# Kernel optimization log

Measured on AMD Instinct MI355X. Metric: run time of the kernel, lower is better.

The kernel has to match this reference:

```python
import jax, jax.numpy as jnp
import numpy as np

B, C, H, W = 2, 256, 64, 64
HEADS = 8
HEAD_DIM = C // HEADS  # 32
INNER = HEADS * HEAD_DIM  # 256
GROUPS = 32
EPS = 1e-5


def groupnorm(x, w, b):
    # x: [B, C, H, W]; normalize over (C//G, H, W) within each of G groups
    Bx, Cx, Hx, Wx = x.shape
    xg = x.reshape(Bx, GROUPS, -1)
    mu = xg.mean(axis=-1, keepdims=True)
    var = xg.var(axis=-1, keepdims=True)
    xn = ((xg - mu) * jax.lax.rsqrt(var + EPS)).reshape(Bx, Cx, Hx, Wx)
    return xn * w[:, None, None] + b[:, None, None]


def setup_inputs() -> dict:
    key = jax.random.key(0)
    k0, k1, k2 = jax.random.split(key, 3)
    x = jax.random.normal(k0, (B, C, H, W), dtype=jnp.float32)
    gn_weight = jnp.ones((C,), dtype=jnp.float32)
    gn_bias = jnp.zeros((C,), dtype=jnp.float32)
    # 1x1 conv weights (kernel dims squeezed): [out_ch, in_ch]
    w_qkv = jax.random.normal(k1, (3 * INNER, C), dtype=jnp.float32) * 0.02
    w_out = jax.random.normal(k2, (C, INNER), dtype=jnp.float32) * 0.02
    return {"x": x, "gn_weight": gn_weight, "gn_bias": gn_bias,
            "w_qkv": w_qkv, "w_out": w_out}


def reference(x, gn_weight, gn_bias, w_qkv, w_out):
    Bx, Cx, Hx, Wx = x.shape
    N = Hx * Wx
    scale = HEAD_DIM ** -0.5
    xn = groupnorm(x, gn_weight, gn_bias)
    # 1x1 conv == channel matmul
    qkv = jnp.einsum('oc,bchw->bohw', w_qkv, xn)  # [B, 3*INNER, H, W]
    q, k, v = jnp.split(qkv, 3, axis=1)
    # 'b (h d) x y -> b h (x y) d'
    def to_heads(t):
        return t.reshape(Bx, HEADS, HEAD_DIM, N).transpose(0, 1, 3, 2)  # bhnd
    q, k, v = to_heads(q), to_heads(k), to_heads(v)
    sim = jnp.einsum('bhid,bhjd->bhij', q, k) * scale  # [B, h, N, N]
    attn = jax.nn.softmax(sim, axis=-1)
    o = jnp.einsum('bhij,bhjd->bhid', attn, v)  # [B, h, N, d]
    # 'b h (x y) d -> b (h d) x y'
    o = o.transpose(0, 1, 3, 2).reshape(Bx, INNER, Hx, Wx)
    out = jnp.einsum('co,bohw->bchw', w_out, o)
    return x + out
```

## Files before the change

### kernel.cpp

```cpp
#include <hip/hip_runtime.h>
#include <hip/hip_bf16.h>

#define BATCH 2
#define CH 256
#define HW 4096
#define HEADS 8
#define HDIM 32
#define GROUPS 32
#define EPS 1e-5f
#define SCALE 0.17677669529663687f
#define QSCALE (0.17677669529663687f * 1.4426950408889634f)

typedef short s16x8 __attribute__((ext_vector_type(8)));
typedef float floatx4 __attribute__((ext_vector_type(4)));
typedef unsigned short ushort_t;
typedef unsigned int uint_t;

static __device__ __forceinline__ ushort_t f2bf(float f) {
    __hip_bfloat16 h = __float2bfloat16(f);
    return *reinterpret_cast<ushort_t*>(&h);
}
static __device__ __forceinline__ float bf2f(uint_t u) {
    return __uint_as_float(u << 16);
}

static __device__ __forceinline__ uint_t pk2(float lo, float hi) {
    return __builtin_amdgcn_perm(__float_as_uint(hi), __float_as_uint(lo), 0x07060302u);
}

static __device__ __forceinline__ void gload_lds16(const ushort_t* g, ushort_t* l) {
    __builtin_amdgcn_global_load_lds((const __attribute__((address_space(1))) void*)g,
                                     (__attribute__((address_space(3))) void*)l, 16, 0, 0);
}

__global__ void gn_stats_wcvt(const float* __restrict__ x, float* __restrict__ stats,
                              const float* __restrict__ wq, const float* __restrict__ wo,
                              ushort_t* __restrict__ wdst) {
    if (blockIdx.x >= 64) {
        int i = (blockIdx.x - 64) * 256 + threadIdx.x;
        float4 v = (i < 49152) ? ((const float4*)wq)[i] : ((const float4*)wo)[i - 49152];
        ushort_t p[4] = {f2bf(v.x), f2bf(v.y), f2bf(v.z), f2bf(v.w)};
        uint2 o;
        o.x = (uint_t)p[0] | ((uint_t)p[1] << 16);
        o.y = (uint_t)p[2] | ((uint_t)p[3] << 16);
        *(uint2*)&wdst[(size_t)i * 4] = o;
        return;
    }
    int bg = blockIdx.x;
    const float4* xv = (const float4*)(x + (size_t)bg * 8 * HW);
    int t = threadIdx.x;
    float s = 0.f, ss = 0.f;
    for (int i = t; i < 8192; i += 256) {
        float4 v = xv[i];
        s  += v.x + v.y + v.z + v.w;
        ss += v.x*v.x + v.y*v.y + v.z*v.z + v.w*v.w;
    }
    #pragma unroll
    for (int off = 32; off; off >>= 1) {
        s  += __shfl_down(s, off);
        ss += __shfl_down(ss, off);
    }
    __shared__ float rs[4], rss[4];
    int wave = t >> 6;
    if ((t & 63) == 0) { rs[wave] = s; rss[wave] = ss; }
    __syncthreads();
    if (t == 0) {
        s  = rs[0] + rs[1] + rs[2] + rs[3];
        ss = rss[0] + rss[1] + rss[2] + rss[3];
        float mu  = s / 32768.f;
        float var = ss / 32768.f - mu * mu;
        stats[bg * 2]     = mu;
        stats[bg * 2 + 1] = rsqrtf(var + EPS);
    }
}

__global__ void norm_transpose(const float* __restrict__ x, const float* __restrict__ stats,
                               const float* __restrict__ gw, const float* __restrict__ gb,
                               ushort_t* __restrict__ xn) {
    __shared__ ushort_t tile[64][40];
    int b = blockIdx.z, c0 = blockIdx.y * 32, n0 = blockIdx.x * 64;
    int t = threadIdx.x;
    #pragma unroll
    for (int i = 0; i < 8; i++) {
        int idx = i * 256 + t;
        int c = idx >> 6, n = idx & 63;
        int cc = c0 + c;
        float mu   = stats[(b * GROUPS + (cc >> 3)) * 2];
        float rstd = stats[(b * GROUPS + (cc >> 3)) * 2 + 1];
        float v = x[((size_t)b * CH + cc) * HW + n0 + n];
        v = (v - mu) * rstd * gw[cc] + gb[cc];
        tile[n][c] = f2bf(v);
    }
    __syncthreads();
    int n = t >> 2, chk = t & 3;
    uint4 val = *(const uint4*)&tile[n][chk * 8];
    *(uint4*)(xn + ((size_t)(b * HW + n0 + n)) * CH + c0 + chk * 8) = val;
}

__global__ void qkv_gemm(const ushort_t* __restrict__ xn, const ushort_t* __restrict__ wqb,
                         ushort_t* __restrict__ qo, ushort_t* __restrict__ ko,
                         ushort_t* __restrict__ vo) {
    __shared__ ushort_t Al[64][40];
    __shared__ ushort_t Bl[128][40];
    int b = blockIdx.z;
    int n0 = blockIdx.x * 64, o0 = blockIdx.y * 128;
    int t = threadIdx.x, lane = t & 63, wave = t >> 6;
    int lr = lane & 15, lk = lane >> 4;
    int row = t >> 2, chk = t & 3;
    const ushort_t* asrc = xn + ((size_t)(b * HW + n0 + row)) * CH + chk * 8;
    int s1 = t + 256;
    const ushort_t* bsrc0 = wqb + (size_t)(o0 + (t >> 2)) * CH + (t & 3) * 8;
    const ushort_t* bsrc1 = wqb + (size_t)(o0 + (s1 >> 2)) * CH + (s1 & 3) * 8;
    floatx4 acc[8] = {};
    uint4 ra  = *(const uint4*)(asrc);
    uint4 rb0 = *(const uint4*)(bsrc0);
    uint4 rb1 = *(const uint4*)(bsrc1);
    for (int k0 = 0; k0 < 8; k0++) {
        *(uint4*)&Al[row][chk * 8] = ra;
        *(uint4*)&Bl[t >> 2][(t & 3) * 8] = rb0;
        *(uint4*)&Bl[s1 >> 2][(s1 & 3) * 8] = rb1;
        __syncthreads();
        if (k0 < 7) {
            ra  = *(const uint4*)(asrc + (k0 + 1) * 32);
            rb0 = *(const uint4*)(bsrc0 + (k0 + 1) * 32);
            rb1 = *(const uint4*)(bsrc1 + (k0 + 1) * 32);
        }
        s16x8 af = *(const s16x8*)&Al[wave * 16 + lr][lk * 8];
        #pragma unroll
        for (int ct = 0; ct < 8; ct++) {
            s16x8 bf = *(const s16x8*)&Bl[ct * 16 + lr][lk * 8];
            acc[ct] = __builtin_amdgcn_mfma_f32_16x16x32_bf16(af, bf, acc[ct], 0, 0, 0);
        }
        __syncthreads();
    }
    #pragma unroll
    for (int ct = 0; ct < 8; ct++) {
        int o = o0 + ct * 16 + lr;
        int sel = o >> 8;
        int h = (o >> 5) & 7;
        int d = o & 31;
        int nrow0 = n0 + wave * 16 + (lk << 2);
        if (sel == 0) {
            #pragma unroll
            for (int r = 0; r < 4; r++)
                qo[(((size_t)(b * HEADS + h)) * HW + nrow0 + r) * HDIM + d] =
                    f2bf(acc[ct][r] * QSCALE);
        } else if (sel == 1) {
            #pragma unroll
            for (int r = 0; r < 4; r++) {
                int tt = (nrow0 + r) & 63;
                int sg = 4 * ((tt >> 3) & 3) + 16 * ((((tt >> 2) & 1) << 1) | ((tt >> 5) & 1)) + (tt & 3);
                ko[(((size_t)(b * HEADS + h)) * HW + n0 + sg) * HDIM + d] = f2bf(acc[ct][r]);
            }
        } else {
            ushort_t pk[4];
            #pragma unroll
            for (int r = 0; r < 4; r++) pk[r] = f2bf(acc[ct][r]);
            *(uint2*)&vo[(((size_t)(b * HEADS + h)) * HDIM + d) * HW + nrow0] = *(uint2*)pk;
        }
    }
}

__global__ void __launch_bounds__(256, 4)
attn13(const ushort_t* __restrict__ qg, const ushort_t* __restrict__ kg,
       const ushort_t* __restrict__ vg, ushort_t* __restrict__ op0,
       ushort_t* __restrict__ op1, float* __restrict__ lpart) {
    __shared__ ushort_t Kl[2][2048];
    __shared__ ushort_t Vl[2][2048];
    const int bh = blockIdx.y;
    const int z = blockIdx.z;
    const int n0 = blockIdx.x * 128;
    const int t = threadIdx.x;
    const int lane = t & 63, w = t >> 6;
    const int lr = lane & 15, lk = lane >> 4;

    const ushort_t* kb = kg + (size_t)bh * HW * HDIM + (size_t)z * 1024 * HDIM;
    const ushort_t* vb = vg + (size_t)bh * HDIM * HW + z * 1024;

    const int lrr = t & 15, lkk = (t >> 4) & 3, wv = t >> 6;
    const ushort_t* gk = kb + ((wv << 4) + lrr) * HDIM + lkk * 8;
    const ushort_t* gv = vb + (size_t)(((t >> 7) << 4) + lrr) * HW + ((t >> 6) & 1) * 32 + lkk * 8;
    ushort_t* kd0 = &Kl[0][wv << 9]; ushort_t* kd1 = &Kl[1][wv << 9];
    ushort_t* vd0 = &Vl[0][wv << 9]; ushort_t* vd1 = &Vl[1][wv << 9];

    s16x8 qf0 = *(const s16x8*)(qg + ((size_t)bh * HW + n0 + w * 16 + lr) * HDIM + lk * 8);
    s16x8 qf1 = *(const s16x8*)(qg + ((size_t)bh * HW + n0 + 64 + w * 16 + lr) * HDIM + lk * 8);

    const s16x8 onesf = {0x3F80, 0x3F80, 0x3F80, 0x3F80, 0x3F80, 0x3F80, 0x3F80, 0x3F80};
    const floatx4 zf = {};
    floatx4 oacc[2][2] = {};
    floatx4 Lacc[2] = {};

    auto stage = [&](ushort_t* kdn, ushort_t* vdn) {
        gload_lds16(gk, kdn);
        gload_lds16(gv, vdn);
        gk += 64 * HDIM; gv += 64;
    };
    auto compute = [&](const ushort_t* Kb, const ushort_t* Vb) {
        floatx4 sim0[4], sim1[4];
        __builtin_amdgcn_s_setprio(1);
#pragma unroll
        for (int ct = 0; ct < 4; ct++) {
            s16x8 kf = *(const s16x8*)(Kb + ct * 512 + lane * 8);
            sim0[ct] = __builtin_amdgcn_mfma_f32_16x16x32_bf16(kf, qf0, zf, 0, 0, 0);
            sim1[ct] = __builtin_amdgcn_mfma_f32_16x16x32_bf16(kf, qf1, zf, 0, 0, 0);
        }
        __builtin_amdgcn_s_setprio(0);
        s16x8 vf[4];
#pragma unroll
        for (int i = 0; i < 4; i++)
            vf[i] = *(const s16x8*)(Vb + i * 512 + lane * 8);
        {
            s16x8 pf[2];
#pragma unroll
            for (int s = 0; s < 2; s++) {
                union { uint_t u[4]; s16x8 v; } pu;
                pu.u[0] = pk2(__builtin_amdgcn_exp2f(sim0[s][0]),     __builtin_amdgcn_exp2f(sim0[s][1]));
                pu.u[1] = pk2(__builtin_amdgcn_exp2f(sim0[s][2]),     __builtin_amdgcn_exp2f(sim0[s][3]));
                pu.u[2] = pk2(__builtin_amdgcn_exp2f(sim0[s + 2][0]), __builtin_amdgcn_exp2f(sim0[s + 2][1]));
                pu.u[3] = pk2(__builtin_amdgcn_exp2f(sim0[s + 2][2]), __builtin_amdgcn_exp2f(sim0[s + 2][3]));
                pf[s] = pu.v;
            }
            __builtin_amdgcn_s_setprio(1);
#pragma unroll
            for (int s = 0; s < 2; s++) {
                oacc[0][0] = __builtin_amdgcn_mfma_f32_16x16x32_bf16(vf[s],     pf[s], oacc[0][0], 0, 0, 0);
                oacc[0][1] = __builtin_amdgcn_mfma_f32_16x16x32_bf16(vf[2 + s], pf[s], oacc[0][1], 0, 0, 0);
                Lacc[0]    = __builtin_amdgcn_mfma_f32_16x16x32_bf16(onesf,     pf[s], Lacc[0],    0, 0, 0);
            }
            __builtin_amdgcn_s_setprio(0);
        }
        {
            s16x8 pf[2];
#pragma unroll
            for (int s = 0; s < 2; s++) {
                union { uint_t u[4]; s16x8 v; } pu;
                pu.u[0] = pk2(__builtin_amdgcn_exp2f(sim1[s][0]),     __builtin_amdgcn_exp2f(sim1[s][1]));
                pu.u[1] = pk2(__builtin_amdgcn_exp2f(sim1[s][2]),     __builtin_amdgcn_exp2f(sim1[s][3]));
                pu.u[2] = pk2(__builtin_amdgcn_exp2f(sim1[s + 2][0]), __builtin_amdgcn_exp2f(sim1[s + 2][1]));
                pu.u[3] = pk2(__builtin_amdgcn_exp2f(sim1[s + 2][2]), __builtin_amdgcn_exp2f(sim1[s + 2][3]));
                pf[s] = pu.v;
            }
            __builtin_amdgcn_s_setprio(1);
#pragma unroll
            for (int s = 0; s < 2; s++) {
                oacc[1][0] = __builtin_amdgcn_mfma_f32_16x16x32_bf16(vf[s],     pf[s], oacc[1][0], 0, 0, 0);
                oacc[1][1] = __builtin_amdgcn_mfma_f32_16x16x32_bf16(vf[2 + s], pf[s], oacc[1][1], 0, 0, 0);
                Lacc[1]    = __builtin_amdgcn_mfma_f32_16x16x32_bf16(onesf,     pf[s], Lacc[1],    0, 0, 0);
            }
            __builtin_amdgcn_s_setprio(0);
        }
    };

    stage(kd0, vd0);
    __syncthreads();
    for (int s2 = 0; s2 < 8; s2++) {
        stage(kd1, vd1);
        compute(&Kl[0][0], &Vl[0][0]);
        __syncthreads();
        if (s2 < 7) {
            stage(kd0, vd0);
            compute(&Kl[1][0], &Vl[1][0]);
            __syncthreads();
        } else {
            compute(&Kl[1][0], &Vl[1][0]);
        }
    }

    ushort_t* ob = (z == 0 ? op0 : op1 + (size_t)(z - 1) * 2097152) + ((size_t)bh * HW) * 32;
    float* lp = lpart + (size_t)(z * 16 + bh) * HW;
#pragma unroll
    for (int c = 0; c < 2; c++) {
        int n = n0 + c * 64 + w * 16 + lr;
        if (lk == 0) lp[n] = Lacc[c][0];
#pragma unroll
        for (int ct2 = 0; ct2 < 2; ct2++) {
            uint_t lo = (uint_t)f2bf(oacc[c][ct2][0]) | ((uint_t)f2bf(oacc[c][ct2][1]) << 16);
            uint_t hi = (uint_t)f2bf(oacc[c][ct2][2]) | ((uint_t)f2bf(oacc[c][ct2][3]) << 16);
            uint2 val = {lo, hi};
            *(uint2*)(ob + (size_t)n * 32 + ct2 * 16 + lk * 4) = val;
        }
    }
}

__global__ void attn_merge(const ushort_t* __restrict__ op0, const ushort_t* __restrict__ op1,
                           const float* __restrict__ lpart, ushort_t* __restrict__ oa) {
    int idx = blockIdx.x * 256 + threadIdx.x;
    int chunk = idx & 3;
    int n = (idx >> 2) & 4095;
    int bh = idx >> 14;
    size_t base = ((size_t)bh * HW + n) * 32 + chunk * 8;
    uint4 a0 = *(const uint4*)(op0 + base);
    uint4 a1 = *(const uint4*)(op1 + base);
    uint4 a2 = *(const uint4*)(op1 + 2097152 + base);
    uint4 a3 = *(const uint4*)(op1 + 2 * 2097152 + base);
    float L = lpart[(size_t)bh * HW + n] + lpart[(size_t)(16 + bh) * HW + n] +
              lpart[(size_t)(32 + bh) * HW + n] + lpart[(size_t)(48 + bh) * HW + n];
    float inv = 1.0f / L;
    uint_t u0[4] = {a0.x, a0.y, a0.z, a0.w}, u1[4] = {a1.x, a1.y, a1.z, a1.w};
    uint_t u2[4] = {a2.x, a2.y, a2.z, a2.w}, u3[4] = {a3.x, a3.y, a3.z, a3.w};
    ushort_t res[8];
#pragma unroll
    for (int i = 0; i < 4; i++) {
        float lo = bf2f(u0[i] & 0xffffu) + bf2f(u1[i] & 0xffffu) +
                   bf2f(u2[i] & 0xffffu) + bf2f(u3[i] & 0xffffu);
        float hi = bf2f(u0[i] >> 16) + bf2f(u1[i] >> 16) +
                   bf2f(u2[i] >> 16) + bf2f(u3[i] >> 16);
        res[2 * i]     = f2bf(lo * inv);
        res[2 * i + 1] = f2bf(hi * inv);
    }
    ushort_t* dst = oa + ((size_t)((bh >> 3) * HW) + n) * CH + (bh & 7) * 32 + chunk * 8;
    *(uint4*)dst = *(uint4*)res;
}

__global__ void proj_res(const ushort_t* __restrict__ oa, const ushort_t* __restrict__ wob,
                         const float* __restrict__ x, float* __restrict__ out) {
    __shared__ ushort_t Al[64][40];
    __shared__ ushort_t Bl[64][40];
    int m0 = blockIdx.x * 64;
    int c0 = blockIdx.y * 64;
    int t = threadIdx.x, lane = t & 63, wave = t >> 6;
    int lr = lane & 15, lk = lane >> 4;
    int row = t >> 2, chk = t & 3;
    const ushort_t* asrc = oa + (size_t)(m0 + row) * CH + chk * 8;
    const ushort_t* bsrc = wob + (size_t)(c0 + row) * CH + chk * 8;
    floatx4 acc[4] = {};
    uint4 ra = *(const uint4*)(asrc);
    uint4 rb = *(const uint4*)(bsrc);
    for (int k0 = 0; k0 < 8; k0++) {
        *(uint4*)&Al[row][chk * 8] = ra;
        *(uint4*)&Bl[row][chk * 8] = rb;
        __syncthreads();
        if (k0 < 7) {
            ra = *(const uint4*)(asrc + (k0 + 1) * 32);
            rb = *(const uint4*)(bsrc + (k0 + 1) * 32);
        }
        s16x8 af = *(const s16x8*)&Al[wave * 16 + lr][lk * 8];
        #pragma unroll
        for (int ct = 0; ct < 4; ct++) {
            s16x8 bf = *(const s16x8*)&Bl[ct * 16 + lr][lk * 8];
            acc[ct] = __builtin_amdgcn_mfma_f32_16x16x32_bf16(af, bf, acc[ct], 0, 0, 0);
        }
        __syncthreads();
    }
    int mrow0 = m0 + wave * 16 + (lk << 2);
    int b = mrow0 >> 12;
    int n = mrow0 & 4095;
    #pragma unroll
    for (int ct = 0; ct < 4; ct++) {
        int c = c0 + ct * 16 + lr;
        const float4 xv = *(const float4*)(x + ((size_t)(b * CH + c)) * HW + n);
        float4 ov;
        ov.x = acc[ct][0] + xv.x;
        ov.y = acc[ct][1] + xv.y;
        ov.z = acc[ct][2] + xv.z;
        ov.w = acc[ct][3] + xv.w;
        *(float4*)(out + ((size_t)(b * CH + c)) * HW + n) = ov;
    }
}

extern "C" void kernel_launch(void* const* d_in, const int* in_sizes, int n_in,
                              void* d_out, int out_size, void* d_ws, size_t ws_size,
                              hipStream_t stream) {
    const float* x    = (const float*)d_in[0];
    const float* gw   = (const float*)d_in[1];
    const float* gb   = (const float*)d_in[2];
    const float* wqkv = (const float*)d_in[3];
    const float* wout = (const float*)d_in[4];
    float* out = (float*)d_out;

    char* ws = (char*)d_ws;
    float* stats = (float*)ws;
    ushort_t* xn = (ushort_t*)(ws + 512);
    size_t per = (size_t)BATCH * HW * CH;
    ushort_t* q   = xn + per;
    ushort_t* k   = q + per;
    ushort_t* v   = k + per;
    ushort_t* oa  = v + per;
    ushort_t* wqb = oa + per;
    ushort_t* wob = wqb + 196608;
    ushort_t* op1 = wob + 65536;
    float* lpart  = (float*)(op1 + 3 * 2097152);
    ushort_t* op0 = xn;

    gn_stats_wcvt<<<320, 256, 0, stream>>>(x, stats, wqkv, wout, wqb);
    norm_transpose<<<dim3(64, 8, 2), 256, 0, stream>>>(x, stats, gw, gb, xn);
    qkv_gemm<<<dim3(64, 6, 2), 256, 0, stream>>>(xn, wqb, q, k, v);
    attn13<<<dim3(32, 16, 4), 256, 0, stream>>>(q, k, v, op0, op1, lpart);
    attn_merge<<<1024, 256, 0, stream>>>(op0, op1, lpart, oa);
    proj_res<<<dim3(128, 4), 256, 0, stream>>>(oa, wob, x, out);
}
```

Baseline: 85.02 us.

## Software-pipeline QK^T of next tile with softmax and PV of previous tile

Splits the attention inner step into a consume phase (QK^T MFMAs plus the V fragment loads from LDS) and a softmaxPV phase (exp2, packing, PV MFMAs). The loop is restructured so the QK^T for one K/V tile is issued while the exp and PV work of the previous tile is still pending. The intent is to overlap the transcendental ALU work with matrix-core work inside a wave. Keeping two sets of sim and V fragments raises register pressure, so launch bounds drop from 4 to 3 blocks per SIMD, which costs occupancy.

```diff
diff --git a/kernel.cpp b/kernel.cpp
--- a/kernel.cpp
+++ b/kernel.cpp
@@ -161,8 +161,8 @@
     }
 }
 
-__global__ void __launch_bounds__(256, 4)
-attn13(const ushort_t* __restrict__ qg, const ushort_t* __restrict__ kg,
+__global__ void __launch_bounds__(256, 3)
+attn14(const ushort_t* __restrict__ qg, const ushort_t* __restrict__ kg,
        const ushort_t* __restrict__ vg, ushort_t* __restrict__ op0,
        ushort_t* __restrict__ op1, float* __restrict__ lpart) {
     __shared__ ushort_t Kl[2][2048];
@@ -190,82 +190,71 @@
     const floatx4 zf = {};
     floatx4 oacc[2][2] = {};
     floatx4 Lacc[2] = {};
+    floatx4 simA[2][4], simB[2][4];
+    s16x8 vfA[4], vfB[4];
 
     auto stage = [&](ushort_t* kdn, ushort_t* vdn) {
         gload_lds16(gk, kdn);
         gload_lds16(gv, vdn);
         gk += 64 * HDIM; gv += 64;
     };
-    auto compute = [&](const ushort_t* Kb, const ushort_t* Vb) {
-        floatx4 sim0[4], sim1[4];
+    auto consume = [&](const ushort_t* Kb, const ushort_t* Vb,
+                       floatx4 (&sim)[2][4], s16x8 (&vf)[4]) {
         __builtin_amdgcn_s_setprio(1);
 #pragma unroll
         for (int ct = 0; ct < 4; ct++) {
             s16x8 kf = *(const s16x8*)(Kb + ct * 512 + lane * 8);
-            sim0[ct] = __builtin_amdgcn_mfma_f32_16x16x32_bf16(kf, qf0, zf, 0, 0, 0);
-            sim1[ct] = __builtin_amdgcn_mfma_f32_16x16x32_bf16(kf, qf1, zf, 0, 0, 0);
+            sim[0][ct] = __builtin_amdgcn_mfma_f32_16x16x32_bf16(kf, qf0, zf, 0, 0, 0);
+            sim[1][ct] = __builtin_amdgcn_mfma_f32_16x16x32_bf16(kf, qf1, zf, 0, 0, 0);
         }
         __builtin_amdgcn_s_setprio(0);
-        s16x8 vf[4];
 #pragma unroll
         for (int i = 0; i < 4; i++)
             vf[i] = *(const s16x8*)(Vb + i * 512 + lane * 8);
-        {
+    };
+    auto softmaxPV = [&](floatx4 (&sim)[2][4], s16x8 (&vf)[4]) {
+#pragma unroll
+        for (int c = 0; c < 2; c++) {
             s16x8 pf[2];
 #pragma unroll
             for (int s = 0; s < 2; s++) {
                 union { uint_t u[4]; s16x8 v; } pu;
-                pu.u[0] = pk2(__builtin_amdgcn_exp2f(sim0[s][0]),     __builtin_amdgcn_exp2f(sim0[s][1]));
-                pu.u[1] = pk2(__builtin_amdgcn_exp2f(sim0[s][2]),     __builtin_amdgcn_exp2f(sim0[s][3]));
-                pu.u[2] = pk2(__builtin_amdgcn_exp2f(sim0[s + 2][0]), __builtin_amdgcn_exp2f(sim0[s + 2][1]));
-                pu.u[3] = pk2(__builtin_amdgcn_exp2f(sim0[s + 2][2]), __builtin_amdgcn_exp2f(sim0[s + 2][3]));
+                pu.u[0] = pk2(__builtin_amdgcn_exp2f(sim[c][s][0]),     __builtin_amdgcn_exp2f(sim[c][s][1]));
+                pu.u[1] = pk2(__builtin_amdgcn_exp2f(sim[c][s][2]),     __builtin_amdgcn_exp2f(sim[c][s][3]));
+                pu.u[2] = pk2(__builtin_amdgcn_exp2f(sim[c][s + 2][0]), __builtin_amdgcn_exp2f(sim[c][s + 2][1]));
+                pu.u[3] = pk2(__builtin_amdgcn_exp2f(sim[c][s + 2][2]), __builtin_amdgcn_exp2f(sim[c][s + 2][3]));
                 pf[s] = pu.v;
             }
             __builtin_amdgcn_s_setprio(1);
 #pragma unroll
             for (int s = 0; s < 2; s++) {
-                oacc[0][0] = __builtin_amdgcn_mfma_f32_16x16x32_bf16(vf[s],     pf[s], oacc[0][0], 0, 0, 0);
-                oacc[0][1] = __builtin_amdgcn_mfma_f32_16x16x32_bf16(vf[2 + s], pf[s], oacc[0][1], 0, 0, 0);
-                Lacc[0]    = __builtin_amdgcn_mfma_f32_16x16x32_bf16(onesf,     pf[s], Lacc[0],    0, 0, 0);
+                oacc[c][0] = __builtin_amdgcn_mfma_f32_16x16x32_bf16(vf[s],     pf[s], oacc[c][0], 0, 0, 0);
+                oacc[c][1] = __builtin_amdgcn_mfma_f32_16x16x32_bf16(vf[2 + s], pf[s], oacc[c][1], 0, 0, 0);
+                Lacc[c]    = __builtin_amdgcn_mfma_f32_16x16x32_bf16(onesf,     pf[s], Lacc[c],    0, 0, 0);
             }
             __builtin_amdgcn_s_setprio(0);
         }
-        {
-            s16x8 pf[2];
-#pragma unroll
-            for (int s = 0; s < 2; s++) {
-                union { uint_t u[4]; s16x8 v; } pu;
-                pu.u[0] = pk2(__builtin_amdgcn_exp2f(sim1[s][0]),     __builtin_amdgcn_exp2f(sim1[s][1]));
-                pu.u[1] = pk2(__builtin_amdgcn_exp2f(sim1[s][2]),     __builtin_amdgcn_exp2f(sim1[s][3]));
-                pu.u[2] = pk2(__builtin_amdgcn_exp2f(sim1[s + 2][0]), __builtin_amdgcn_exp2f(sim1[s + 2][1]));
-                pu.u[3] = pk2(__builtin_amdgcn_exp2f(sim1[s + 2][2]), __builtin_amdgcn_exp2f(sim1[s + 2][3]));
-                pf[s] = pu.v;
-            }
-            __builtin_amdgcn_s_setprio(1);
-#pragma unroll
-            for (int s = 0; s < 2; s++) {
-                oacc[1][0] = __builtin_amdgcn_mfma_f32_16x16x32_bf16(vf[s],     pf[s], oacc[1][0], 0, 0, 0);
-                oacc[1][1] = __builtin_amdgcn_mfma_f32_16x16x32_bf16(vf[2 + s], pf[s], oacc[1][1], 0, 0, 0);
-                Lacc[1]    = __builtin_amdgcn_mfma_f32_16x16x32_bf16(onesf,     pf[s], Lacc[1],    0, 0, 0);
-            }
-            __builtin_amdgcn_s_setprio(0);
-        }
     };
 
     stage(kd0, vd0);
     __syncthreads();
-    for (int s2 = 0; s2 < 8; s2++) {
+    consume(&Kl[0][0], &Vl[0][0], simA, vfA);
+    stage(kd1, vd1);
+
+    for (int j = 0; j < 7; j++) {
+        __syncthreads();
+        consume(&Kl[1][0], &Vl[1][0], simB, vfB);
+        stage(kd0, vd0);
+        softmaxPV(simA, vfA);
+        __syncthreads();
+        consume(&Kl[0][0], &Vl[0][0], simA, vfA);
         stage(kd1, vd1);
-        compute(&Kl[0][0], &Vl[0][0]);
-        __syncthreads();
-        if (s2 < 7) {
-            stage(kd0, vd0);
-            compute(&Kl[1][0], &Vl[1][0]);
-            __syncthreads();
-        } else {
-            compute(&Kl[1][0], &Vl[1][0]);
-        }
-    }
+        softmaxPV(simB, vfB);
+    }
+    __syncthreads();
+    consume(&Kl[1][0], &Vl[1][0], simB, vfB);
+    softmaxPV(simA, vfA);
+    softmaxPV(simB, vfB);
 
     ushort_t* ob = (z == 0 ? op0 : op1 + (size_t)(z - 1) * 2097152) + ((size_t)bh * HW) * 32;
     float* lp = lpart + (size_t)(z * 16 + bh) * HW;
@@ -386,7 +375,7 @@
     gn_stats_wcvt<<<320, 256, 0, stream>>>(x, stats, wqkv, wout, wqb);
     norm_transpose<<<dim3(64, 8, 2), 256, 0, stream>>>(x, stats, gw, gb, xn);
     qkv_gemm<<<dim3(64, 6, 2), 256, 0, stream>>>(xn, wqb, q, k, v);
-    attn13<<<dim3(32, 16, 4), 256, 0, stream>>>(q, k, v, op0, op1, lpart);
+    attn14<<<dim3(32, 16, 4), 256, 0, stream>>>(q, k, v, op0, op1, lpart);
     attn_merge<<<1024, 256, 0, stream>>>(op0, op1, lpart, oa);
     proj_res<<<dim3(128, 4), 256, 0, stream>>>(oa, wob, x, out);
 }
```

Measured after the change: 88.78 us. +4.4%, slower.
